# Performance work log

Measured on AMD Instinct MI355X. Metric: run time of the kernel, lower is better.

The kernel has to match this reference:

```python
import jax, jax.numpy as jnp
import numpy as np

B = 65536      # batch
N_IN = 784     # n_input_neurons
D = 10         # n_neurons_per_hidd_bank
NB = 10        # banks per layer (layer0 = input banks 0-9, layer1 = output banks 10-19)
N_OUT = 10     # n_output_neurons
N_HIDD_BANKS = 20


def setup_inputs() -> dict:
    key = jax.random.key(0)
    ks = jax.random.split(key, 10)
    s_in = 1.0 / np.sqrt(N_IN)
    s_d = 1.0 / np.sqrt(D)
    return {
        "x": jax.random.normal(ks[0], (B, N_IN), dtype=jnp.float32),
        # input-bank linears: 784 -> 10, one per input bank
        "W_in": jax.random.uniform(ks[1], (NB, N_IN, D), jnp.float32, -s_in, s_in),
        "b_in": jax.random.uniform(ks[2], (NB, D), jnp.float32, -s_in, s_in),
        # gate linears per (source, target) connection: 10 -> 1
        "W_gate": jax.random.uniform(ks[3], (NB, NB, D), jnp.float32, -s_d, s_d),
        "b_gate": jax.random.uniform(ks[4], (NB, NB), jnp.float32, -s_d, s_d),
        # data linears per (source, target) connection: 10 -> 10
        "W_data": jax.random.uniform(ks[5], (NB, NB, D, D), jnp.float32, -s_d, s_d),
        "b_data": jax.random.uniform(ks[6], (NB, NB, D), jnp.float32, -s_d, s_d),
        # output-bank linears: 10 -> 10, one per output bank
        "W_out": jax.random.uniform(ks[7], (NB, D, N_OUT), jnp.float32, -s_d, s_d),
        "b_out": jax.random.uniform(ks[8], (NB, N_OUT), jnp.float32, -s_d, s_d),
    }


def reference(x, W_in, b_in, W_gate, b_gate, W_data, b_data, W_out, b_out):
    # Input banks (banks 0-9): relu(Linear_784->10)
    acts0 = jax.nn.relu(jnp.einsum("bi,sid->sbd", x, W_in) + b_in[:, None, :])  # [S,B,D]

    # Gates: original checks gate_act.data[0,0] > 0, i.e. scalar from batch row 0 only.
    gate = jnp.einsum("sd,std->st", acts0[:, 0, :], W_gate) + b_gate  # [S,T]
    mask = (gate > 0.0).astype(x.dtype)                               # [S,T] binary, detached

    # Per-connection data linears (bias included per open connection, as in original)
    data = jnp.einsum("sbd,stde->stbe", acts0, W_data) + b_data[:, :, None, :]  # [S,T,B,D]
    target_pre = jnp.einsum("st,stbe->tbe", mask, data)                          # [T,B,D]
    acts1 = jax.nn.relu(target_pre)                                              # [T,B,D]

    # A target bank is active (non-None) iff any incoming gate is open; its output
    # linear (including bias) only contributes when active.
    any_open = (jnp.sum(mask, axis=0) > 0.0).astype(x.dtype)  # [T]
    out_contrib = jnp.einsum("tbe,teo->tbo", acts1, W_out) + b_out[:, None, :]
    logits = jnp.einsum("t,tbo->bo", any_open, out_contrib)   # [B,N_OUT]

    output = jax.nn.log_softmax(logits, axis=1)
    prob_open_gate = jnp.sum(mask) / N_HIDD_BANKS
    return output, prob_open_gate
```

## Files before the change

### kernel.cpp

```cpp
#include <hip/hip_runtime.h>
#include <math.h>

#define BATCH   65536
#define N_IN    784
#define DD      10
#define NB      10
#define SD      100
#define N_OUTS  10
#define TILES   16
#define ROWST   16
#define XSTRIDE 1616
#define XBUFB   (16 * XSTRIDE)

typedef float  f32x4  __attribute__((ext_vector_type(4)));
typedef short  bf16x8 __attribute__((ext_vector_type(8)));

#define WTF_F 0
#define WDF_F 51200
#define WOF_F 59392
#define BD_F  60416
#define BL_F  60544

__device__ __forceinline__ short f2bf(float f) {
    unsigned u = __builtin_bit_cast(unsigned, f);
    unsigned r = u + 0x7fffu + ((u >> 16) & 1u);
    return (short)(r >> 16);
}

#define BAR_LGKM() do {                                          \
    asm volatile("s_waitcnt lgkmcnt(0)" ::: "memory");           \
    __builtin_amdgcn_s_barrier();                                \
    __builtin_amdgcn_sched_barrier(0); } while (0)

__global__ __launch_bounds__(1024) void prep_kernel(
                             const float* __restrict__ x,
                             const float* __restrict__ W_in,
                             const float* __restrict__ b_in,
                             const float* __restrict__ W_gate,
                             const float* __restrict__ b_gate,
                             const float* __restrict__ W_data,
                             const float* __restrict__ b_data,
                             const float* __restrict__ W_out,
                             const float* __restrict__ b_out,
                             float* __restrict__ out,
                             float* __restrict__ ws) {
    const int tid = threadIdx.x;

    if (blockIdx.x != 0) {
        short* wtf = (short*)(ws + WTF_F);
        int idx = (int)(blockIdx.x - 1) * 1024 + tid;
        if (idx < 25 * 8 * 512) {
            int K = idx / 4096, rem = idx % 4096;
            int ct = rem / 512, l2 = rem % 512;
            int l = l2 >> 3, e = l2 & 7;
            int r = l & 15, g = l >> 4;
            int c = 16 * ct + r, k = K * 32 + g * 8 + e;
            float v = (c < SD && k < N_IN)
                          ? W_in[(c / DD) * (N_IN * DD) + k * DD + (c % DD)] : 0.f;
            wtf[idx] = f2bf(v);
        }
        return;
    }

    __shared__ float a0r0[SD];
    __shared__ float mask_l[SD];
    __shared__ float ao_l[NB];

    if (tid < 800) {
        int c = tid >> 3, h = tid & 7;
        int s = c / DD, d = c % DD;
        const float* wcol = W_in + s * (N_IN * DD) + d;
        float acc = 0.f;
        int i0 = h * 98;
        #pragma unroll 14
        for (int i = i0; i < i0 + 98; ++i)
            acc += x[i] * wcol[i * DD];
        acc += __shfl_xor(acc, 1, 64);
        acc += __shfl_xor(acc, 2, 64);
        acc += __shfl_xor(acc, 4, 64);
        if (h == 0) a0r0[c] = fmaxf(acc + b_in[c], 0.f);
    }
    __syncthreads();

    if (tid < SD) {
        float g = b_gate[tid];
        int s = tid / DD;
        for (int d = 0; d < DD; ++d)
            g += a0r0[s * DD + d] * W_gate[tid * DD + d];
        mask_l[tid] = (g > 0.f) ? 1.f : 0.f;
    }
    __syncthreads();

    if (tid < NB) {
        float any = 0.f;
        for (int s = 0; s < NB; ++s) any = fmaxf(any, mask_l[s * DD + tid]);
        ao_l[tid] = any;
    }
    if (tid == 0) {
        float sum = 0.f;
        for (int i = 0; i < SD; ++i) sum += mask_l[i];
        out[(long)BATCH * N_OUTS] = sum / 20.0f;
    }
    __syncthreads();

    {
        short* wdf = (short*)(ws + WDF_F);
        for (int idx = tid; idx < 4 * 8 * 512; idx += 1024) {
            int kk = idx / 4096, rem = idx % 4096;
            int ct = rem / 512, l2 = rem % 512;
            int l = l2 >> 3, e = l2 & 7;
            int r = l & 15, g = l >> 4;
            int m = 16 * ct + r, k = kk * 32 + g * 8 + e;
            float v = 0.f;
            if (m < SD && k < SD) {
                int t = m / DD, eo = m % DD, s = k / DD, d = k % DD;
                v = mask_l[s * DD + t] * W_data[((s * NB + t) * DD + d) * DD + eo];
            }
            wdf[idx] = f2bf(v);
        }
    }
    {
        short* wof = (short*)(ws + WOF_F);
        for (int idx = tid; idx < 4 * 512; idx += 1024) {
            int kk = idx / 512, l2 = idx % 512;
            int l = l2 >> 3, e = l2 & 7;
            int o = l & 15, g = l >> 4;
            int te = kk * 32 + g * 8 + e;
            float v = 0.f;
            if (o < 10 && te < SD) {
                int t = te / DD, eo = te % DD;
                v = ao_l[t] * W_out[(t * DD + eo) * N_OUTS + o];
            }
            wof[idx] = f2bf(v);
        }
    }
    if (tid < 128) {
        float v = 0.f;
        if (tid < SD) {
            int t = tid / DD, e = tid % DD;
            for (int s = 0; s < NB; ++s)
                v += mask_l[s * DD + t] * b_data[(s * NB + t) * DD + e];
        }
        ws[BD_F + tid] = v;
    }
    if (tid < N_OUTS) {
        float v = 0.f;
        for (int t = 0; t < NB; ++t) v += ao_l[t] * b_out[t * N_OUTS + tid];
        ws[BL_F + tid] = v;
    }
}

__global__ __launch_bounds__(512, 1) void main_kernel(
        const float* __restrict__ x,
        const float* __restrict__ b_in,
        const float* __restrict__ ws,
        float* __restrict__ out) {
    __shared__ __align__(16) unsigned char xb16[2][XBUFB];
    __shared__ __align__(16) short a0b[2][16 * 136];
    __shared__ __align__(16) short a1b[2][16 * 136];

    const int tid  = threadIdx.x;
    const int w    = tid >> 6;
    const int lane = tid & 63;
    const int g    = lane >> 4;
    const int r    = lane & 15;
    const size_t rowbase = (size_t)blockIdx.x * (TILES * ROWST);
    const float4* xblk = (const float4*)(x + rowbase * N_IN);

    const short* wtf = (const short*)(ws + WTF_F);
    const short* wdf = (const short*)(ws + WDF_F);
    const short* wof = (const short*)(ws + WOF_F);

    int loff[7];
    #pragma unroll
    for (int q = 0; q < 7; ++q) {
        int idx = tid + 512 * q;
        int row = idx / 196, col = idx - row * 196;
        if (row > 15) row = 15;
        loff[q] = row * XSTRIDE + col * 8;
    }

    bf16x8 wt[25];
    #pragma unroll
    for (int K = 0; K < 25; ++K)
        wt[K] = *(const bf16x8*)(wtf + (K * 8 + w) * 512 + lane * 8);
    bf16x8 wd[4], wo[4];
    #pragma unroll
    for (int kk = 0; kk < 4; ++kk) {
        wd[kk] = *(const bf16x8*)(wdf + (kk * 8 + w) * 512 + lane * 8);
        wo[kk] = *(const bf16x8*)(wof + kk * 512 + lane * 8);
    }
    float bi[4], bd[4], blv[4];
    #pragma unroll
    for (int j = 0; j < 4; ++j) {
        int c = 16 * w + 4 * g + j;
        bi[j] = (c < SD) ? b_in[c] : 0.f;
        bd[j] = ws[BD_F + c];
        int o = 4 * g + j;
        blv[j] = (o < 10) ? ws[BL_F + o] : 0.f;
    }

    float4 xr[7];

#define STAGE_LOAD(t) do {                                                     \
    const float4* _s = xblk + (size_t)(t) * 3136;                              \
    _Pragma("unroll")                                                          \
    for (int _q = 0; _q < 6; ++_q)                                             \
        xr[_q] = _s[tid + 512 * _q];                                           \
    if (tid < 64) xr[6] = _s[tid + 3072];                                      \
    __builtin_amdgcn_sched_barrier(0);                                         \
} while (0)

#define STAGE_WRITE(bufp) do {                                                 \
    _Pragma("unroll")                                                          \
    for (int _q = 0; _q < 6; ++_q) {                                           \
        unsigned _u0, _u1;                                                     \
        asm("v_cvt_pk_bf16_f32 %0, %1, %2"                                     \
            : "=v"(_u0) : "v"(xr[_q].x), "v"(xr[_q].y));                       \
        asm("v_cvt_pk_bf16_f32 %0, %1, %2"                                     \
            : "=v"(_u1) : "v"(xr[_q].z), "v"(xr[_q].w));                       \
        *(uint2*)((bufp) + loff[_q]) = make_uint2(_u0, _u1);                   \
    }                                                                          \
    if (tid < 64) {                                                            \
        unsigned _u0, _u1;                                                     \
        asm("v_cvt_pk_bf16_f32 %0, %1, %2"                                     \
            : "=v"(_u0) : "v"(xr[6].x), "v"(xr[6].y));                         \
        asm("v_cvt_pk_bf16_f32 %0, %1, %2"                                     \
            : "=v"(_u1) : "v"(xr[6].z), "v"(xr[6].w));                         \
        *(uint2*)((bufp) + loff[6]) = make_uint2(_u0, _u1);                    \
    }                                                                          \
} while (0)

    STAGE_LOAD(0);
    for (int i = tid; i < 192; i += 512) {
        int buf = i / 96, rem = i - buf * 96;
        int row = rem / 6, p = rem - row * 6;
        *(uint2*)(&xb16[buf][0] + row * XSTRIDE + 1568 + p * 8) = make_uint2(0u, 0u);
    }
    STAGE_WRITE(&xb16[0][0]);
    BAR_LGKM();

    for (int t = 0; t < TILES; ++t) {
        const int cur = t & 1;
        if (t + 1 < TILES) STAGE_LOAD(t + 1);

        {
            f32x4 acc = (f32x4){0.f, 0.f, 0.f, 0.f};
            const unsigned char* xbr = &xb16[cur][0] + r * XSTRIDE + g * 16;
            #pragma unroll
            for (int K = 0; K < 25; ++K) {
                bf16x8 bf = *(const bf16x8*)(xbr + K * 64);
                acc = __builtin_amdgcn_mfma_f32_16x16x32_bf16(wt[K], bf, acc, 0, 0, 0);
            }
            short* myrow = &a0b[cur][0] + r * 136;
            int c0 = 16 * w + 4 * g;
            float v0 = fmaxf(acc[0] + bi[0], 0.f), v1 = fmaxf(acc[1] + bi[1], 0.f);
            float v2 = fmaxf(acc[2] + bi[2], 0.f), v3 = fmaxf(acc[3] + bi[3], 0.f);
            unsigned p01, p23;
            asm("v_cvt_pk_bf16_f32 %0, %1, %2" : "=v"(p01) : "v"(v0), "v"(v1));
            asm("v_cvt_pk_bf16_f32 %0, %1, %2" : "=v"(p23) : "v"(v2), "v"(v3));
            *(uint2*)(myrow + c0) = make_uint2(p01, p23);
        }
        BAR_LGKM();

        {
            f32x4 acc2 = (f32x4){0.f, 0.f, 0.f, 0.f};
            #pragma unroll
            for (int kk = 0; kk < 4; ++kk) {
                bf16x8 bf = *(const bf16x8*)(&a0b[cur][0] + r * 136 + kk * 32 + g * 8);
                acc2 = __builtin_amdgcn_mfma_f32_16x16x32_bf16(wd[kk], bf, acc2, 0, 0, 0);
            }
            short* myrow = &a1b[cur][0] + r * 136;
            int c0 = 16 * w + 4 * g;
            float v0 = fmaxf(acc2[0] + bd[0], 0.f), v1 = fmaxf(acc2[1] + bd[1], 0.f);
            float v2 = fmaxf(acc2[2] + bd[2], 0.f), v3 = fmaxf(acc2[3] + bd[3], 0.f);
            unsigned p01, p23;
            asm("v_cvt_pk_bf16_f32 %0, %1, %2" : "=v"(p01) : "v"(v0), "v"(v1));
            asm("v_cvt_pk_bf16_f32 %0, %1, %2" : "=v"(p23) : "v"(v2), "v"(v3));
            *(uint2*)(myrow + c0) = make_uint2(p01, p23);
        }
        if (t + 1 < TILES) STAGE_WRITE(&xb16[cur ^ 1][0]);
        BAR_LGKM();

        {
            f32x4 accL = (f32x4){0.f, 0.f, 0.f, 0.f};
            #pragma unroll
            for (int kk = 0; kk < 4; ++kk) {
                bf16x8 bf = *(const bf16x8*)(&a1b[cur][0] + r * 136 + kk * 32 + g * 8);
                accL = __builtin_amdgcn_mfma_f32_16x16x32_bf16(wo[kk], bf, accL, 0, 0, 0);
            }
            float lgf[4];
            #pragma unroll
            for (int j = 0; j < 4; ++j)
                lgf[j] = (4 * g + j < 10) ? accL[j] + blv[j] : -1e30f;

            float m = fmaxf(fmaxf(lgf[0], lgf[1]), fmaxf(lgf[2], lgf[3]));
            m = fmaxf(m, __shfl_xor(m, 16, 64));
            m = fmaxf(m, __shfl_xor(m, 32, 64));
            float s = expf(lgf[0] - m) + expf(lgf[1] - m)
                    + expf(lgf[2] - m) + expf(lgf[3] - m);
            s += __shfl_xor(s, 16, 64);
            s += __shfl_xor(s, 32, 64);
            float z = m + logf(s);

            if ((r >> 1) == w) {
                float* ob = out + (rowbase + (size_t)t * ROWST + r) * N_OUTS + 4 * g;
                if (g < 3) *(float2*)(ob)     = make_float2(lgf[0] - z, lgf[1] - z);
                if (g < 2) *(float2*)(ob + 2) = make_float2(lgf[2] - z, lgf[3] - z);
            }
        }
    }
#undef STAGE_LOAD
#undef STAGE_WRITE
}

extern "C" void kernel_launch(void* const* d_in, const int* in_sizes, int n_in,
                              void* d_out, int out_size, void* d_ws, size_t ws_size,
                              hipStream_t stream) {
    const float* x      = (const float*)d_in[0];
    const float* W_in   = (const float*)d_in[1];
    const float* b_in   = (const float*)d_in[2];
    const float* W_gate = (const float*)d_in[3];
    const float* b_gate = (const float*)d_in[4];
    const float* W_data = (const float*)d_in[5];
    const float* b_data = (const float*)d_in[6];
    const float* W_out  = (const float*)d_in[7];
    const float* b_out  = (const float*)d_in[8];
    float* out = (float*)d_out;
    float* ws  = (float*)d_ws;

    prep_kernel<<<257, 1024, 0, stream>>>(x, W_in, b_in, W_gate, b_gate,
                                          W_data, b_data, W_out, b_out, out, ws);
    main_kernel<<<256, 512, 0, stream>>>(x, b_in, ws, out);
}
```

Before: 68.17 us.

## Specialize warps into producer loaders and MFMA consumers with deeper prefetch

Adds four producer wavefronts (768 threads per block) that handle all global x loads and bf16 conversion into shared memory, while the original eight wavefronts only run the MFMA stages. Producers prefetch two tiles ahead. The data and output weights move from registers into shared memory, and the a0/a1 buffers lose their double buffering. The aim is to separate memory latency from compute and free consumer registers, at the cost of extra LDS reads per tile and a larger block. The launch_bounds min-blocks value of 3 may force tighter register limits.

```diff
diff --git a/kernel.cpp b/kernel.cpp
--- a/kernel.cpp
+++ b/kernel.cpp
@@ -150,14 +150,16 @@
     }
 }
 
-__global__ __launch_bounds__(512, 1) void main_kernel(
+__global__ __launch_bounds__(768, 3) void main_kernel(
         const float* __restrict__ x,
         const float* __restrict__ b_in,
         const float* __restrict__ ws,
         float* __restrict__ out) {
     __shared__ __align__(16) unsigned char xb16[2][XBUFB];
-    __shared__ __align__(16) short a0b[2][16 * 136];
-    __shared__ __align__(16) short a1b[2][16 * 136];
+    __shared__ __align__(16) short a0b[16 * 136];
+    __shared__ __align__(16) short a1b[16 * 136];
+    __shared__ __align__(16) short wdL[4 * 8 * 512];
+    __shared__ __align__(16) short woL[4 * 512];
 
     const int tid  = threadIdx.x;
     const int w    = tid >> 6;
@@ -171,80 +173,80 @@
     const short* wdf = (const short*)(ws + WDF_F);
     const short* wof = (const short*)(ws + WOF_F);
 
-    int loff[7];
-    #pragma unroll
-    for (int q = 0; q < 7; ++q) {
-        int idx = tid + 512 * q;
-        int row = idx / 196, col = idx - row * 196;
-        if (row > 15) row = 15;
-        loff[q] = row * XSTRIDE + col * 8;
+    for (int idx = tid; idx < 4 * 8 * 512; idx += 768) wdL[idx] = wdf[idx];
+    for (int idx = tid; idx < 4 * 512; idx += 768)     woL[idx] = wof[idx];
+    for (int i = tid; i < 192; i += 768) {
+        int buf = i / 96, rem = i - buf * 96;
+        int row = rem / 6, p = rem - row * 6;
+        *(uint2*)(&xb16[buf][0] + row * XSTRIDE + 1568 + p * 8) = make_uint2(0u, 0u);
     }
 
     bf16x8 wt[25];
-    #pragma unroll
-    for (int K = 0; K < 25; ++K)
-        wt[K] = *(const bf16x8*)(wtf + (K * 8 + w) * 512 + lane * 8);
-    bf16x8 wd[4], wo[4];
-    #pragma unroll
-    for (int kk = 0; kk < 4; ++kk) {
-        wd[kk] = *(const bf16x8*)(wdf + (kk * 8 + w) * 512 + lane * 8);
-        wo[kk] = *(const bf16x8*)(wof + kk * 512 + lane * 8);
-    }
     float bi[4], bd[4], blv[4];
-    #pragma unroll
-    for (int j = 0; j < 4; ++j) {
-        int c = 16 * w + 4 * g + j;
-        bi[j] = (c < SD) ? b_in[c] : 0.f;
-        bd[j] = ws[BD_F + c];
-        int o = 4 * g + j;
-        blv[j] = (o < 10) ? ws[BL_F + o] : 0.f;
-    }
-
-    float4 xr[7];
+    if (w < 8) {
+        #pragma unroll
+        for (int K = 0; K < 25; ++K)
+            wt[K] = *(const bf16x8*)(wtf + (K * 8 + w) * 512 + lane * 8);
+        #pragma unroll
+        for (int j = 0; j < 4; ++j) {
+            int c = 16 * w + 4 * g + j;
+            bi[j] = (c < SD) ? b_in[c] : 0.f;
+            bd[j] = ws[BD_F + c];
+            int o = 4 * g + j;
+            blv[j] = (o < 10) ? ws[BL_F + o] : 0.f;
+        }
+    }
+
+    const int ptid = (w >= 8) ? (tid - 512) : 0;
+    int loff[13];
+    float4 xr[13];
+    if (w >= 8) {
+        #pragma unroll
+        for (int q = 0; q < 13; ++q) {
+            int idx = ptid + 256 * q;
+            if (idx < 3136) {
+                int row = idx / 196, col = idx - row * 196;
+                loff[q] = row * XSTRIDE + col * 8;
+            } else loff[q] = 0;
+        }
+    }
 
 #define STAGE_LOAD(t) do {                                                     \
     const float4* _s = xblk + (size_t)(t) * 3136;                              \
     _Pragma("unroll")                                                          \
-    for (int _q = 0; _q < 6; ++_q)                                             \
-        xr[_q] = _s[tid + 512 * _q];                                           \
-    if (tid < 64) xr[6] = _s[tid + 3072];                                      \
+    for (int _q = 0; _q < 13; ++_q) {                                          \
+        int _idx = ptid + 256 * _q;                                            \
+        if (_idx < 3136) xr[_q] = _s[_idx];                                    \
+    }                                                                          \
     __builtin_amdgcn_sched_barrier(0);                                         \
 } while (0)
 
 #define STAGE_WRITE(bufp) do {                                                 \
     _Pragma("unroll")                                                          \
-    for (int _q = 0; _q < 6; ++_q) {                                           \
-        unsigned _u0, _u1;                                                     \
-        asm("v_cvt_pk_bf16_f32 %0, %1, %2"                                     \
-            : "=v"(_u0) : "v"(xr[_q].x), "v"(xr[_q].y));                       \
-        asm("v_cvt_pk_bf16_f32 %0, %1, %2"                                     \
-            : "=v"(_u1) : "v"(xr[_q].z), "v"(xr[_q].w));                       \
-        *(uint2*)((bufp) + loff[_q]) = make_uint2(_u0, _u1);                   \
-    }                                                                          \
-    if (tid < 64) {                                                            \
-        unsigned _u0, _u1;                                                     \
-        asm("v_cvt_pk_bf16_f32 %0, %1, %2"                                     \
-            : "=v"(_u0) : "v"(xr[6].x), "v"(xr[6].y));                         \
-        asm("v_cvt_pk_bf16_f32 %0, %1, %2"                                     \
-            : "=v"(_u1) : "v"(xr[6].z), "v"(xr[6].w));                         \
-        *(uint2*)((bufp) + loff[6]) = make_uint2(_u0, _u1);                    \
+    for (int _q = 0; _q < 13; ++_q) {                                          \
+        int _idx = ptid + 256 * _q;                                            \
+        if (_idx < 3136) {                                                     \
+            unsigned _u0, _u1;                                                 \
+            asm("v_cvt_pk_bf16_f32 %0, %1, %2"                                 \
+                : "=v"(_u0) : "v"(xr[_q].x), "v"(xr[_q].y));                   \
+            asm("v_cvt_pk_bf16_f32 %0, %1, %2"                                 \
+                : "=v"(_u1) : "v"(xr[_q].z), "v"(xr[_q].w));                   \
+            *(uint2*)((bufp) + loff[_q]) = make_uint2(_u0, _u1);               \
+        }                                                                      \
     }                                                                          \
 } while (0)
 
-    STAGE_LOAD(0);
-    for (int i = tid; i < 192; i += 512) {
-        int buf = i / 96, rem = i - buf * 96;
-        int row = rem / 6, p = rem - row * 6;
-        *(uint2*)(&xb16[buf][0] + row * XSTRIDE + 1568 + p * 8) = make_uint2(0u, 0u);
-    }
-    STAGE_WRITE(&xb16[0][0]);
+    if (w >= 8) {
+        STAGE_LOAD(0);
+        STAGE_WRITE(&xb16[0][0]);
+        STAGE_LOAD(1);
+    }
     BAR_LGKM();
 
     for (int t = 0; t < TILES; ++t) {
         const int cur = t & 1;
-        if (t + 1 < TILES) STAGE_LOAD(t + 1);
-
-        {
+
+        if (w < 8) {
             f32x4 acc = (f32x4){0.f, 0.f, 0.f, 0.f};
             const unsigned char* xbr = &xb16[cur][0] + r * XSTRIDE + g * 16;
             #pragma unroll
@@ -252,7 +254,7 @@
                 bf16x8 bf = *(const bf16x8*)(xbr + K * 64);
                 acc = __builtin_amdgcn_mfma_f32_16x16x32_bf16(wt[K], bf, acc, 0, 0, 0);
             }
-            short* myrow = &a0b[cur][0] + r * 136;
+            short* myrow = a0b + r * 136;
             int c0 = 16 * w + 4 * g;
             float v0 = fmaxf(acc[0] + bi[0], 0.f), v1 = fmaxf(acc[1] + bi[1], 0.f);
             float v2 = fmaxf(acc[2] + bi[2], 0.f), v3 = fmaxf(acc[3] + bi[3], 0.f);
@@ -263,14 +265,15 @@
         }
         BAR_LGKM();
 
-        {
+        if (w < 8) {
             f32x4 acc2 = (f32x4){0.f, 0.f, 0.f, 0.f};
             #pragma unroll
             for (int kk = 0; kk < 4; ++kk) {
-                bf16x8 bf = *(const bf16x8*)(&a0b[cur][0] + r * 136 + kk * 32 + g * 8);
-                acc2 = __builtin_amdgcn_mfma_f32_16x16x32_bf16(wd[kk], bf, acc2, 0, 0, 0);
-            }
-            short* myrow = &a1b[cur][0] + r * 136;
+                bf16x8 af = *(const bf16x8*)(wdL + (kk * 8 + w) * 512 + lane * 8);
+                bf16x8 bf = *(const bf16x8*)(a0b + r * 136 + kk * 32 + g * 8);
+                acc2 = __builtin_amdgcn_mfma_f32_16x16x32_bf16(af, bf, acc2, 0, 0, 0);
+            }
+            short* myrow = a1b + r * 136;
             int c0 = 16 * w + 4 * g;
             float v0 = fmaxf(acc2[0] + bd[0], 0.f), v1 = fmaxf(acc2[1] + bd[1], 0.f);
             float v2 = fmaxf(acc2[2] + bd[2], 0.f), v3 = fmaxf(acc2[3] + bd[3], 0.f);
@@ -278,16 +281,19 @@
             asm("v_cvt_pk_bf16_f32 %0, %1, %2" : "=v"(p01) : "v"(v0), "v"(v1));
             asm("v_cvt_pk_bf16_f32 %0, %1, %2" : "=v"(p23) : "v"(v2), "v"(v3));
             *(uint2*)(myrow + c0) = make_uint2(p01, p23);
-        }
-        if (t + 1 < TILES) STAGE_WRITE(&xb16[cur ^ 1][0]);
+        } else {
+            if (t + 1 < TILES) STAGE_WRITE(&xb16[cur ^ 1][0]);
+            if (t + 2 < TILES) STAGE_LOAD(t + 2);
+        }
         BAR_LGKM();
 
-        {
+        if (w < 8) {
             f32x4 accL = (f32x4){0.f, 0.f, 0.f, 0.f};
             #pragma unroll
             for (int kk = 0; kk < 4; ++kk) {
-                bf16x8 bf = *(const bf16x8*)(&a1b[cur][0] + r * 136 + kk * 32 + g * 8);
-                accL = __builtin_amdgcn_mfma_f32_16x16x32_bf16(wo[kk], bf, accL, 0, 0, 0);
+                bf16x8 af = *(const bf16x8*)(woL + kk * 512 + lane * 8);
+                bf16x8 bf = *(const bf16x8*)(a1b + r * 136 + kk * 32 + g * 8);
+                accL = __builtin_amdgcn_mfma_f32_16x16x32_bf16(af, bf, accL, 0, 0, 0);
             }
             float lgf[4];
             #pragma unroll
@@ -331,5 +337,5 @@
 
     prep_kernel<<<257, 1024, 0, stream>>>(x, W_in, b_in, W_gate, b_gate,
                                           W_data, b_data, W_out, b_out, out, ws);
-    main_kernel<<<256, 512, 0, stream>>>(x, b_in, ws, out);
+    main_kernel<<<256, 768, 0, stream>>>(x, b_in, ws, out);
 }
```

Result: slower. 143.9 us (+111.2%).

## Double block to 1024 threads with split-K first GEMM and producer waves

Applied to the files above, without the earlier changes.

Blocks grow to 1024 threads (16 waves). The 784-wide input GEMM is split in K between two 8-wave halves, whose partial sums are combined through LDS. The second half also acts as producer, loading x from global memory and converting it to bf16 in shared memory. The data and output weights move from registers to LDS, and the a0/a1 activation buffers become single-buffered. The aim is more waves in flight to hide latency and lower per-thread register pressure, at the cost of an extra barrier per tile, idle producer waves during the tail stages, and possible register spills from the tighter launch bounds.

```diff
diff --git a/kernel.cpp b/kernel.cpp
--- a/kernel.cpp
+++ b/kernel.cpp
@@ -150,20 +150,25 @@
     }
 }
 
-__global__ __launch_bounds__(512, 1) void main_kernel(
+__global__ __launch_bounds__(1024, 4) void main_kernel(
         const float* __restrict__ x,
         const float* __restrict__ b_in,
         const float* __restrict__ ws,
         float* __restrict__ out) {
     __shared__ __align__(16) unsigned char xb16[2][XBUFB];
-    __shared__ __align__(16) short a0b[2][16 * 136];
-    __shared__ __align__(16) short a1b[2][16 * 136];
+    __shared__ __align__(16) short a0b[16 * 136];
+    __shared__ __align__(16) short a1b[16 * 136];
+    __shared__ __align__(16) short wdL[4 * 8 * 512];
+    __shared__ __align__(16) short woL[4 * 512];
+    __shared__ __align__(16) unsigned char pL[8 * 1024];
 
     const int tid  = threadIdx.x;
     const int w    = tid >> 6;
     const int lane = tid & 63;
     const int g    = lane >> 4;
     const int r    = lane & 15;
+    const int ct   = w & 7;
+    const int kh   = w >> 3;
     const size_t rowbase = (size_t)blockIdx.x * (TILES * ROWST);
     const float4* xblk = (const float4*)(x + rowbase * N_IN);
 
@@ -171,43 +176,53 @@
     const short* wdf = (const short*)(ws + WDF_F);
     const short* wof = (const short*)(ws + WOF_F);
 
+    for (int idx = tid; idx < 4 * 8 * 512; idx += 1024) wdL[idx] = wdf[idx];
+    for (int idx = tid; idx < 4 * 512; idx += 1024)     woL[idx] = wof[idx];
+    for (int i = tid; i < 192; i += 1024) {
+        int buf = i / 96, rem = i - buf * 96;
+        int row = rem / 6, p = rem - row * 6;
+        *(uint2*)(&xb16[buf][0] + row * XSTRIDE + 1568 + p * 8) = make_uint2(0u, 0u);
+    }
+
+    bf16x8 wt[13];
+    const int k0 = kh * 13;
+    #pragma unroll
+    for (int i = 0; i < 13; ++i) {
+        int K = k0 + i;
+        if (K > 24) K = 24;
+        wt[i] = *(const bf16x8*)(wtf + (K * 8 + ct) * 512 + lane * 8);
+    }
+    float bi[4], bd[4], blv[4];
+    if (kh == 0) {
+        #pragma unroll
+        for (int j = 0; j < 4; ++j) {
+            int c = 16 * ct + 4 * g + j;
+            bi[j] = (c < SD) ? b_in[c] : 0.f;
+            bd[j] = ws[BD_F + c];
+            int o = 4 * g + j;
+            blv[j] = (o < 10) ? ws[BL_F + o] : 0.f;
+        }
+    }
+
+    const int ptid = tid - 512;
     int loff[7];
-    #pragma unroll
-    for (int q = 0; q < 7; ++q) {
-        int idx = tid + 512 * q;
-        int row = idx / 196, col = idx - row * 196;
-        if (row > 15) row = 15;
-        loff[q] = row * XSTRIDE + col * 8;
-    }
-
-    bf16x8 wt[25];
-    #pragma unroll
-    for (int K = 0; K < 25; ++K)
-        wt[K] = *(const bf16x8*)(wtf + (K * 8 + w) * 512 + lane * 8);
-    bf16x8 wd[4], wo[4];
-    #pragma unroll
-    for (int kk = 0; kk < 4; ++kk) {
-        wd[kk] = *(const bf16x8*)(wdf + (kk * 8 + w) * 512 + lane * 8);
-        wo[kk] = *(const bf16x8*)(wof + kk * 512 + lane * 8);
-    }
-    float bi[4], bd[4], blv[4];
-    #pragma unroll
-    for (int j = 0; j < 4; ++j) {
-        int c = 16 * w + 4 * g + j;
-        bi[j] = (c < SD) ? b_in[c] : 0.f;
-        bd[j] = ws[BD_F + c];
-        int o = 4 * g + j;
-        blv[j] = (o < 10) ? ws[BL_F + o] : 0.f;
-    }
-
     float4 xr[7];
+    if (kh == 1) {
+        #pragma unroll
+        for (int q = 0; q < 7; ++q) {
+            int idx = ptid + 512 * q;
+            int row = idx / 196, col = idx - row * 196;
+            if (row > 15) { row = 15; col = 0; }
+            loff[q] = row * XSTRIDE + col * 8;
+        }
+    }
 
 #define STAGE_LOAD(t) do {                                                     \
     const float4* _s = xblk + (size_t)(t) * 3136;                              \
     _Pragma("unroll")                                                          \
     for (int _q = 0; _q < 6; ++_q)                                             \
-        xr[_q] = _s[tid + 512 * _q];                                           \
-    if (tid < 64) xr[6] = _s[tid + 3072];                                      \
+        xr[_q] = _s[ptid + 512 * _q];                                          \
+    if (ptid < 64) xr[6] = _s[ptid + 3072];                                    \
     __builtin_amdgcn_sched_barrier(0);                                         \
 } while (0)
 
@@ -221,7 +236,7 @@
             : "=v"(_u1) : "v"(xr[_q].z), "v"(xr[_q].w));                       \
         *(uint2*)((bufp) + loff[_q]) = make_uint2(_u0, _u1);                   \
     }                                                                          \
-    if (tid < 64) {                                                            \
+    if (ptid < 64) {                                                           \
         unsigned _u0, _u1;                                                     \
         asm("v_cvt_pk_bf16_f32 %0, %1, %2"                                     \
             : "=v"(_u0) : "v"(xr[6].x), "v"(xr[6].y));                         \
@@ -231,31 +246,44 @@
     }                                                                          \
 } while (0)
 
-    STAGE_LOAD(0);
-    for (int i = tid; i < 192; i += 512) {
-        int buf = i / 96, rem = i - buf * 96;
-        int row = rem / 6, p = rem - row * 6;
-        *(uint2*)(&xb16[buf][0] + row * XSTRIDE + 1568 + p * 8) = make_uint2(0u, 0u);
-    }
-    STAGE_WRITE(&xb16[0][0]);
+    if (kh == 1) {
+        STAGE_LOAD(0);
+        STAGE_WRITE(&xb16[0][0]);
+    }
     BAR_LGKM();
 
     for (int t = 0; t < TILES; ++t) {
         const int cur = t & 1;
-        if (t + 1 < TILES) STAGE_LOAD(t + 1);
-
+        if (kh == 1 && t + 1 < TILES) STAGE_LOAD(t + 1);
+
+        f32x4 acc = (f32x4){0.f, 0.f, 0.f, 0.f};
         {
-            f32x4 acc = (f32x4){0.f, 0.f, 0.f, 0.f};
             const unsigned char* xbr = &xb16[cur][0] + r * XSTRIDE + g * 16;
-            #pragma unroll
-            for (int K = 0; K < 25; ++K) {
-                bf16x8 bf = *(const bf16x8*)(xbr + K * 64);
-                acc = __builtin_amdgcn_mfma_f32_16x16x32_bf16(wt[K], bf, acc, 0, 0, 0);
-            }
-            short* myrow = &a0b[cur][0] + r * 136;
-            int c0 = 16 * w + 4 * g;
-            float v0 = fmaxf(acc[0] + bi[0], 0.f), v1 = fmaxf(acc[1] + bi[1], 0.f);
-            float v2 = fmaxf(acc[2] + bi[2], 0.f), v3 = fmaxf(acc[3] + bi[3], 0.f);
+            if (kh == 0) {
+                #pragma unroll
+                for (int i = 0; i < 13; ++i) {
+                    bf16x8 bf = *(const bf16x8*)(xbr + i * 64);
+                    acc = __builtin_amdgcn_mfma_f32_16x16x32_bf16(wt[i], bf, acc, 0, 0, 0);
+                }
+            } else {
+                #pragma unroll
+                for (int i = 0; i < 12; ++i) {
+                    bf16x8 bf = *(const bf16x8*)(xbr + (13 + i) * 64);
+                    acc = __builtin_amdgcn_mfma_f32_16x16x32_bf16(wt[i], bf, acc, 0, 0, 0);
+                }
+                *(f32x4*)(pL + ct * 1024 + lane * 16) = acc;
+            }
+        }
+        BAR_LGKM();
+
+        if (kh == 0) {
+            f32x4 p = *(const f32x4*)(pL + ct * 1024 + lane * 16);
+            short* myrow = a0b + r * 136;
+            int c0 = 16 * ct + 4 * g;
+            float v0 = fmaxf(acc[0] + p[0] + bi[0], 0.f);
+            float v1 = fmaxf(acc[1] + p[1] + bi[1], 0.f);
+            float v2 = fmaxf(acc[2] + p[2] + bi[2], 0.f);
+            float v3 = fmaxf(acc[3] + p[3] + bi[3], 0.f);
             unsigned p01, p23;
             asm("v_cvt_pk_bf16_f32 %0, %1, %2" : "=v"(p01) : "v"(v0), "v"(v1));
             asm("v_cvt_pk_bf16_f32 %0, %1, %2" : "=v"(p23) : "v"(v2), "v"(v3));
@@ -263,31 +291,34 @@
         }
         BAR_LGKM();
 
-        {
+        if (kh == 0) {
             f32x4 acc2 = (f32x4){0.f, 0.f, 0.f, 0.f};
             #pragma unroll
             for (int kk = 0; kk < 4; ++kk) {
-                bf16x8 bf = *(const bf16x8*)(&a0b[cur][0] + r * 136 + kk * 32 + g * 8);
-                acc2 = __builtin_amdgcn_mfma_f32_16x16x32_bf16(wd[kk], bf, acc2, 0, 0, 0);
-            }
-            short* myrow = &a1b[cur][0] + r * 136;
-            int c0 = 16 * w + 4 * g;
+                bf16x8 af = *(const bf16x8*)(wdL + (kk * 8 + ct) * 512 + lane * 8);
+                bf16x8 bf = *(const bf16x8*)(a0b + r * 136 + kk * 32 + g * 8);
+                acc2 = __builtin_amdgcn_mfma_f32_16x16x32_bf16(af, bf, acc2, 0, 0, 0);
+            }
+            short* myrow = a1b + r * 136;
+            int c0 = 16 * ct + 4 * g;
             float v0 = fmaxf(acc2[0] + bd[0], 0.f), v1 = fmaxf(acc2[1] + bd[1], 0.f);
             float v2 = fmaxf(acc2[2] + bd[2], 0.f), v3 = fmaxf(acc2[3] + bd[3], 0.f);
             unsigned p01, p23;
             asm("v_cvt_pk_bf16_f32 %0, %1, %2" : "=v"(p01) : "v"(v0), "v"(v1));
             asm("v_cvt_pk_bf16_f32 %0, %1, %2" : "=v"(p23) : "v"(v2), "v"(v3));
             *(uint2*)(myrow + c0) = make_uint2(p01, p23);
-        }
-        if (t + 1 < TILES) STAGE_WRITE(&xb16[cur ^ 1][0]);
+        } else {
+            if (t + 1 < TILES) STAGE_WRITE(&xb16[cur ^ 1][0]);
+        }
         BAR_LGKM();
 
-        {
+        if (kh == 0) {
             f32x4 accL = (f32x4){0.f, 0.f, 0.f, 0.f};
             #pragma unroll
             for (int kk = 0; kk < 4; ++kk) {
-                bf16x8 bf = *(const bf16x8*)(&a1b[cur][0] + r * 136 + kk * 32 + g * 8);
-                accL = __builtin_amdgcn_mfma_f32_16x16x32_bf16(wo[kk], bf, accL, 0, 0, 0);
+                bf16x8 af = *(const bf16x8*)(woL + kk * 512 + lane * 8);
+                bf16x8 bf = *(const bf16x8*)(a1b + r * 136 + kk * 32 + g * 8);
+                accL = __builtin_amdgcn_mfma_f32_16x16x32_bf16(af, bf, accL, 0, 0, 0);
             }
             float lgf[4];
             #pragma unroll
@@ -303,7 +334,7 @@
             s += __shfl_xor(s, 32, 64);
             float z = m + logf(s);
 
-            if ((r >> 1) == w) {
+            if ((r >> 1) == ct) {
                 float* ob = out + (rowbase + (size_t)t * ROWST + r) * N_OUTS + 4 * g;
                 if (g < 3) *(float2*)(ob)     = make_float2(lgf[0] - z, lgf[1] - z);
                 if (g < 2) *(float2*)(ob + 2) = make_float2(lgf[2] - z, lgf[3] - z);
@@ -331,5 +362,5 @@
 
     prep_kernel<<<257, 1024, 0, stream>>>(x, W_in, b_in, W_gate, b_gate,
                                           W_data, b_data, W_out, b_out, out, ws);
-    main_kernel<<<256, 512, 0, stream>>>(x, b_in, ws, out);
+    main_kernel<<<256, 1024, 0, stream>>>(x, b_in, ws, out);
 }
```

New measurement: 70.27 us. 1.03x slower.
